# Performance work log

Measured on AMD Instinct MI355X. Metric: run time of the kernel, lower is better.

The kernel has to match this reference:

```python
import jax, jax.numpy as jnp
import numpy as np

NUM_PATCHES = 16
MAX_WINDOW = 16
PATCH = 4
N_EMBED = 16
T_TOTAL = 16


def _build_indices(T):
    # Replays the nested loops of lcpatchify for a prefix of length T and
    # returns the flat (time, patch) gather indices, concatenated over j.
    pairs = [[(T - 1, j)] for j in range(NUM_PATCHES)]
    i = 2
    for t in range(T - 1, -1, -1):  # reversed(patches[0])
        for j in range(NUM_PATCHES):
            for k in range(-i + 1, i):
                for l in range(-i + 1, i):
                    idx = j + MAX_WINDOW * k + l
                    if not (j == 0 and l == 0 and i == 2) and 0 <= idx < NUM_PATCHES:
                        pairs[j].append((t, idx))
        i += 1
    arr = np.array([p for jl in pairs for p in jl], dtype=np.int32)  # (R_t, 2)
    return arr[:, 0], arr[:, 1]


INDICES = [_build_indices(t + 1) for t in range(T_TOTAL)]
R_TOTAL = sum(len(a) for a, _ in INDICES)


def patchify(imgs, p):
    # Faithful port, including the source's final raw reshape from
    # (B, N, C, p, p) row-major layout into (B, C, N, p*p).
    B, C, H, W = imgs.shape
    h, w = H // p, W // p
    x = imgs.reshape(B, C, h, p, w, p).transpose(0, 2, 4, 1, 3, 5)  # (B,h,w,C,p,p)
    return x.reshape(B, C, h * w, p * p)


def setup_inputs() -> dict:
    key = jax.random.key(0)
    ks = jax.random.split(key, 6)
    s = 1.0 / np.sqrt(N_EMBED)
    return {
        "x": jax.random.normal(ks[0], (1, T_TOTAL, 16, 16), jnp.float32),
        "Wq": jax.random.uniform(ks[1], (N_EMBED, N_EMBED), jnp.float32, -s, s),
        "Wk": jax.random.uniform(ks[2], (NUM_PATCHES, N_EMBED, N_EMBED), jnp.float32, -s, s),
        "bk": jax.random.uniform(ks[3], (NUM_PATCHES, N_EMBED), jnp.float32, -s, s),
        "Wv": jax.random.uniform(ks[4], (NUM_PATCHES, N_EMBED, N_EMBED), jnp.float32, -s, s),
        "bv": jax.random.uniform(ks[5], (NUM_PATCHES, N_EMBED), jnp.float32, -s, s),
    }


def reference(x, Wq, Wk, bk, Wv, bv):
    # q = query Linear (no bias) over patchified x: (1, T, 16, 16)
    q = patchify(x, PATCH) @ Wq.T
    ks, vs = [], []
    for t in range(x.shape[1]):  # fixed structural loop over time steps
        patches = patchify(x[:, : t + 1], PATCH)[0]  # (t+1, 16, 16)
        times, pats = INDICES[t]
        rows = patches[times, pats]                   # ragged gather -> (R_t, 16)
        ks.append(rows @ Wk[t].T + bk[t])             # keys[t] applied to all j windows
        vs.append(rows @ Wv[t].T + bv[t])
    k = jnp.concatenate(ks, axis=0)
    v = jnp.concatenate(vs, axis=0)
    # Single packed output: [q rows; all k rows; all v rows]
    return jnp.concatenate([q.reshape(-1, N_EMBED), k, v], axis=0)
```

## Files before the change

kernel.cpp:

```cpp
#include <hip/hip_runtime.h>
#include <math.h>

#define QROWS 256
#define RT    28528
#define TOTAL (QROWS + 2 * RT)

__global__ __launch_bounds__(256) void head_kernel(
    const float* __restrict__ x,
    const float* __restrict__ Wq,
    const float* __restrict__ Wk,
    const float* __restrict__ bk,
    const float* __restrict__ Wv,
    const float* __restrict__ bv,
    float* __restrict__ out)
{
    __shared__ float sx[4096];
    __shared__ float sWq[256];
    __shared__ float sWk[4096];
    __shared__ float sWv[4096];
    __shared__ float sb[512];

    const int tid = threadIdx.x;
    #pragma unroll
    for (int it = 0; it < 16; ++it) {
        int idx = tid + it * 256;
        sx[idx]  = x[idx];
        sWk[idx] = Wk[idx];
        sWv[idx] = Wv[idx];
    }
    sWq[tid]      = Wq[tid];
    sb[tid]       = bk[tid];
    sb[256 + tid] = bv[tid];
    __syncthreads();

    const int r = blockIdx.x * 256 + tid;
    if (r >= TOTAL) return;

    const int OFF[17] = {0, 63, 206, 461, 860, 1435, 2218, 3241, 4536, 6135,
                         8070, 10373, 13076, 16211, 19810, 23905, 28528};

    int n, c;
    const float* Wmat;
    const float* bvec;
    float bscale;

    if (r < QROWS) {
        n = r >> 4;
        c = r & 15;
        Wmat = sWq;
        bvec = sb;
        bscale = 0.0f;
    } else {
        int rr = r - QROWS;
        int sec = 0;
        if (rr >= RT) { rr -= RT; sec = 1; }

        int g = 0;
        #pragma unroll
        for (int gg = 1; gg < 16; ++gg) g += (rr >= OFF[gg]) ? 1 : 0;
        const int pos = rr - OFF[g];
        const int T = g + 1;
        const int L = (T + 1) * (T + 1);

        int j, p;
        if (pos < L - 1) { j = 0; p = pos; }
        else             { j = (pos + 1) / L; p = (pos + 1) - j * L; }

        int timev, pat;
        if (p == 0) {
            timev = T - 1; pat = j;
        } else {
            int q = p - 1 + ((j == 0) ? 1 : 0);
            int v = q + 1;
            int s = (int)sqrtf((float)v);
            if (s * s > v) --s;
            if ((s + 1) * (s + 1) <= v) ++s;
            const int i = s + 1;
            const int m = v - s * s;
            timev = T + 1 - i;
            int cm = i + j - 16; if (cm < 0) cm = 0;
            if (m < cm) {
                pat = m;
            } else {
                const int m2 = m - cm;
                const int lo0 = (1 - i > -j) ? (1 - i) : (-j);
                const int hi0 = (i - 1 < 15 - j) ? (i - 1) : (15 - j);
                const int c0 = hi0 - lo0 + 1;
                if (m2 < c0) pat = j + lo0 + m2;
                else         pat = j + 17 - i + (m2 - c0);
            }
        }
        const int F = timev * 16 + pat;
        n = F / T;
        c = F - n * T;
        Wmat = (sec ? sWv : sWk) + g * 256;
        bvec = sb + (sec ? 256 : 0) + g * 16;
        bscale = 1.0f;
    }

    const int base = c * 256 + ((n >> 2) << 6) + ((n & 3) << 2);
    float xr[16];
    #pragma unroll
    for (int pr = 0; pr < 4; ++pr) {
        const float4 v4 = *(const float4*)&sx[base + pr * 16];
        xr[pr * 4 + 0] = v4.x; xr[pr * 4 + 1] = v4.y;
        xr[pr * 4 + 2] = v4.z; xr[pr * 4 + 3] = v4.w;
    }

    float o[16];
    #pragma unroll
    for (int e = 0; e < 16; ++e) {
        float acc = bvec[e] * bscale;
        #pragma unroll
        for (int q = 0; q < 16; ++q) acc += xr[q] * Wmat[e * 16 + q];
        o[e] = acc;
    }

    float4* op = (float4*)(out + (size_t)r * 16);
    op[0] = *(float4*)&o[0];
    op[1] = *(float4*)&o[4];
    op[2] = *(float4*)&o[8];
    op[3] = *(float4*)&o[12];
}

extern "C" void kernel_launch(void* const* d_in, const int* in_sizes, int n_in,
                              void* d_out, int out_size, void* d_ws, size_t ws_size,
                              hipStream_t stream) {
    (void)in_sizes; (void)n_in; (void)d_ws; (void)ws_size; (void)out_size;
    const float* x  = (const float*)d_in[0];
    const float* Wq = (const float*)d_in[1];
    const float* Wk = (const float*)d_in[2];
    const float* bk = (const float*)d_in[3];
    const float* Wv = (const float*)d_in[4];
    const float* bv = (const float*)d_in[5];
    float* out = (float*)d_out;
    const int blocks = (TOTAL + 255) / 256;
    head_kernel<<<blocks, 256, 0, stream>>>(x, Wq, Wk, bk, Wv, bv, out);
}
```

Baseline: 67.86 us.

## Assign one weight group per block and stage only its weights and prefix

Measured after the change: 70.95 us. 4.5% more time.

```diff
diff --git a/kernel.cpp b/kernel.cpp
--- a/kernel.cpp
+++ b/kernel.cpp
@@ -3,7 +3,8 @@
 
 #define QROWS 256
 #define RT    28528
-#define TOTAL (QROWS + 2 * RT)
+
+#define NBLOCKS 241
 
 __global__ __launch_bounds__(256) void head_kernel(
     const float* __restrict__ x,
@@ -15,53 +16,55 @@
     float* __restrict__ out)
 {
     __shared__ float sx[4096];
-    __shared__ float sWq[256];
-    __shared__ float sWk[4096];
-    __shared__ float sWv[4096];
-    __shared__ float sb[512];
-
-    const int tid = threadIdx.x;
-    #pragma unroll
-    for (int it = 0; it < 16; ++it) {
-        int idx = tid + it * 256;
-        sx[idx]  = x[idx];
-        sWk[idx] = Wk[idx];
-        sWv[idx] = Wv[idx];
-    }
-    sWq[tid]      = Wq[tid];
-    sb[tid]       = bk[tid];
-    sb[256 + tid] = bv[tid];
-    __syncthreads();
-
-    const int r = blockIdx.x * 256 + tid;
-    if (r >= TOTAL) return;
+    __shared__ float sW[256];
+    __shared__ float sb[16];
 
     const int OFF[17] = {0, 63, 206, 461, 860, 1435, 2218, 3241, 4536, 6135,
                          8070, 10373, 13076, 16211, 19810, 23905, 28528};
 
-    int n, c;
-    const float* Wmat;
-    const float* bvec;
-    float bscale;
+    const int tid = threadIdx.x;
+    const int b = blockIdx.x;
 
-    if (r < QROWS) {
-        n = r >> 4;
-        c = r & 15;
-        Wmat = sWq;
-        bvec = sb;
-        bscale = 0.0f;
+    int g = 0, chunk = 0, sec = 0;
+    const bool isq = (b == 0);
+    if (!isq) {
+        int bb = b - 1;
+        if (bb >= 120) { sec = 1; bb -= 120; }
+        for (int gg = 0; gg < 16; ++gg) {
+            const int nc = (OFF[gg + 1] - OFF[gg] + 255) >> 8;
+            if (bb < nc) { g = gg; chunk = bb; break; }
+            bb -= nc;
+        }
+    }
+    const int T = isq ? 16 : (g + 1);
+
+    for (int it = 0; it < T; ++it) {
+        const int idx = tid + (it << 8);
+        sx[idx] = x[idx];
+    }
+    if (isq) {
+        sW[tid] = Wq[tid];
+        if (tid < 16) sb[tid] = 0.0f;
     } else {
-        int rr = r - QROWS;
-        int sec = 0;
-        if (rr >= RT) { rr -= RT; sec = 1; }
+        sW[tid] = ((sec ? Wv : Wk) + g * 256)[tid];
+        if (tid < 16) sb[tid] = (sec ? bv : bk)[g * 16 + tid];
+    }
+    __syncthreads();
 
-        int g = 0;
-        #pragma unroll
-        for (int gg = 1; gg < 16; ++gg) g += (rr >= OFF[gg]) ? 1 : 0;
-        const int pos = rr - OFF[g];
-        const int T = g + 1;
+    int n, c, row;
+    bool active = true;
+
+    if (isq) {
+        row = tid;
+        n = tid >> 4;
+        c = tid & 15;
+    } else {
+        const int Rg = OFF[g + 1] - OFF[g];
+        int pos = (chunk << 8) + tid;
+        if (pos >= Rg) { active = false; pos = 0; }
+        row = QROWS + sec * RT + OFF[g] + pos;
+
         const int L = (T + 1) * (T + 1);
-
         int j, p;
         if (pos < L - 1) { j = 0; p = pos; }
         else             { j = (pos + 1) / L; p = (pos + 1) - j * L; }
@@ -70,8 +73,8 @@
         if (p == 0) {
             timev = T - 1; pat = j;
         } else {
-            int q = p - 1 + ((j == 0) ? 1 : 0);
-            int v = q + 1;
+            const int qq = p - 1 + ((j == 0) ? 1 : 0);
+            const int v = qq + 1;
             int s = (int)sqrtf((float)v);
             if (s * s > v) --s;
             if ((s + 1) * (s + 1) <= v) ++s;
@@ -93,9 +96,6 @@
         const int F = timev * 16 + pat;
         n = F / T;
         c = F - n * T;
-        Wmat = (sec ? sWv : sWk) + g * 256;
-        bvec = sb + (sec ? 256 : 0) + g * 16;
-        bscale = 1.0f;
     }
 
     const int base = c * 256 + ((n >> 2) << 6) + ((n & 3) << 2);
@@ -110,17 +110,19 @@
     float o[16];
     #pragma unroll
     for (int e = 0; e < 16; ++e) {
-        float acc = bvec[e] * bscale;
+        float acc = sb[e];
         #pragma unroll
-        for (int q = 0; q < 16; ++q) acc += xr[q] * Wmat[e * 16 + q];
+        for (int q = 0; q < 16; ++q) acc += xr[q] * sW[e * 16 + q];
         o[e] = acc;
     }
 
-    float4* op = (float4*)(out + (size_t)r * 16);
-    op[0] = *(float4*)&o[0];
-    op[1] = *(float4*)&o[4];
-    op[2] = *(float4*)&o[8];
-    op[3] = *(float4*)&o[12];
+    if (active) {
+        float4* op = (float4*)(out + (size_t)row * 16);
+        op[0] = *(float4*)&o[0];
+        op[1] = *(float4*)&o[4];
+        op[2] = *(float4*)&o[8];
+        op[3] = *(float4*)&o[12];
+    }
 }
 
 extern "C" void kernel_launch(void* const* d_in, const int* in_sizes, int n_in,
@@ -134,6 +136,5 @@
     const float* Wv = (const float*)d_in[4];
     const float* bv = (const float*)d_in[5];
     float* out = (float*)d_out;
-    const int blocks = (TOTAL + 255) / 256;
-    head_kernel<<<blocks, 256, 0, stream>>>(x, Wq, Wk, bk, Wv, bv, out);
+    head_kernel<<<NBLOCKS, 256, 0, stream>>>(x, Wq, Wk, bk, Wv, bv, out);
 }
```
